# Kernel tuning notes

Hardware: AMD Instinct MI355X
Metric: run time of the kernel (lower is better)

## Reference

```python
import jax, jax.numpy as jnp
import numpy as np

B, T, C = 1, 4096, 1024
N_HEAD = 16
HEAD_DIM = C // N_HEAD
SCALE = 1.0 / np.sqrt(HEAD_DIM).astype(np.float32)


def setup_inputs() -> dict:
    key = jax.random.key(0)
    k1, k2, k3 = jax.random.split(key, 3)
    x = jax.random.normal(k1, (B, T, C), dtype=jnp.float32)
    W_attn = jax.random.normal(k2, (C, 3 * C), dtype=jnp.float32) * 0.02
    b_attn = jnp.zeros((3 * C,), dtype=jnp.float32)
    W_proj = jax.random.normal(k3, (C, C), dtype=jnp.float32) * 0.02
    b_proj = jnp.zeros((C,), dtype=jnp.float32)
    return {"x": x, "W_attn": W_attn, "b_attn": b_attn, "W_proj": W_proj, "b_proj": b_proj}


def reference(x, W_attn, b_attn, W_proj, b_proj):
    Bq, Tq, Cq = x.shape
    qkv = x @ W_attn + b_attn                      # [B, T, 3C]
    q, k, v = jnp.split(qkv, 3, axis=-1)
    # split heads -> [B, H, T, D]
    def split_heads(t):
        return t.reshape(Bq, Tq, N_HEAD, HEAD_DIM).transpose(0, 2, 1, 3)
    q, k, v = split_heads(q), split_heads(k), split_heads(v)
    scores = jnp.einsum('bhqd,bhkd->bhqk', q, k) * SCALE  # [B, H, T, T]
    causal = jnp.tril(jnp.ones((Tq, Tq), dtype=bool))
    scores = jnp.where(causal[None, None], scores, jnp.float32(-jnp.inf))
    probs = jax.nn.softmax(scores, axis=-1)
    out = jnp.einsum('bhqk,bhkd->bhqd', probs, v)          # [B, H, T, D]
    out = out.transpose(0, 2, 1, 3).reshape(Bq, Tq, Cq)    # merge heads
    out = out @ W_proj + b_proj
    return out
```

## Files before the change

### kernel.cpp

```cpp
#include <hip/hip_runtime.h>
#include <hip/hip_bf16.h>


typedef unsigned short u16;
typedef u16 u16x4 __attribute__((ext_vector_type(4)));
typedef u16 u16x8 __attribute__((ext_vector_type(8)));
typedef __bf16 bf16x8 __attribute__((ext_vector_type(8)));
typedef float f32x4 __attribute__((ext_vector_type(4)));

#define T_SEQ 4096
#define C_DIM 1024
#define NH 16
#define HD 64
#define QSC 0.18033688f

static __device__ __forceinline__ u16 f2bf(float f) {
    __hip_bfloat16 h = __float2bfloat16(f);
    return __builtin_bit_cast(u16, h);
}

static __device__ __forceinline__ bf16x8 ldfr(const u16* base, int byteoff) {
    return __builtin_bit_cast(bf16x8, *(const u16x8*)(base + (byteoff >> 1)));
}

static __device__ __forceinline__ void gld_lds16(const void* g, void* l) {
    __builtin_amdgcn_global_load_lds((const __attribute__((address_space(1))) void*)g,
                                     (__attribute__((address_space(3))) void*)l, 16, 0, 0);
}

#define MFMA16(a, b, c) __builtin_amdgcn_mfma_f32_16x16x32_bf16((a), (b), (c), 0, 0, 0)


__global__ __launch_bounds__(256) void k_cvt_x(const float* __restrict__ x, u16* __restrict__ xb) {
    int i = (blockIdx.x * 256 + threadIdx.x) * 8;
    float4 a = *(const float4*)(x + i);
    float4 b = *(const float4*)(x + i + 4);
    u16x8 o;
    o[0] = f2bf(a.x); o[1] = f2bf(a.y); o[2] = f2bf(a.z); o[3] = f2bf(a.w);
    o[4] = f2bf(b.x); o[5] = f2bf(b.y); o[6] = f2bf(b.z); o[7] = f2bf(b.w);
    *(u16x8*)(xb + i) = o;
}

__global__ __launch_bounds__(256) void k_transpose_w(const float* __restrict__ src,
                                                     u16* __restrict__ dst, int R, int Cc) {
    __shared__ float tile[32][33];
    int bx = blockIdx.x * 32;
    int by = blockIdx.y * 32;
    int x = threadIdx.x, y = threadIdx.y;
#pragma unroll
    for (int i = 0; i < 32; i += 8)
        tile[y + i][x] = src[(by + y + i) * Cc + bx + x];
    __syncthreads();
#pragma unroll
    for (int i = 0; i < 32; i += 8)
        dst[(bx + y + i) * R + by + x] = f2bf(tile[x][y + i]);
}


template <int EPI>
__global__ __launch_bounds__(256) void k_gemm(const u16* __restrict__ A, const u16* __restrict__ Bt,
                                              const float* __restrict__ bias,
                                              u16* __restrict__ outQ, u16* __restrict__ outK,
                                              u16* __restrict__ outVt, float* __restrict__ outF,
                                              int kd, int nbx) {
    __shared__ u16 Al[128 * 64];
    __shared__ u16 Bl[128 * 64];
    const int tid = threadIdx.x;
    const int lane = tid & 63;
    const int wid = tid >> 6;
    const int wm = wid >> 1, wn = wid & 1;
    const int c = lane & 15, g = lane >> 4;
    const int nwg = gridDim.x;
    const int swzb = ((int)blockIdx.x & 7) * (nwg >> 3) + ((int)blockIdx.x >> 3);
    const int m0 = (swzb % nbx) * 128;
    const int n0 = (swzb / nbx) * 128;
    const int srow = lane >> 3;
    const int sxu = (((lane & 7) * 16) ^ (srow << 4)) >> 1;
    const int swa = (c & 7) << 4;

    f32x4 acc[4][4] = {};

    for (int k0 = 0; k0 < kd; k0 += 64) {
#pragma unroll
        for (int i = 0; i < 4; ++i) {
            const int ch = wid * 4 + i;
            const int row = ch * 8 + srow;
            gld_lds16(A + (m0 + row) * kd + k0 + sxu, &Al[ch * 512]);
            gld_lds16(Bt + (n0 + row) * kd + k0 + sxu, &Bl[ch * 512]);
        }
        __syncthreads();
        bf16x8 af[4][2], bfm[4][2];
#pragma unroll
        for (int mi = 0; mi < 4; ++mi) {
            const u16* p = Al + (wm * 64 + mi * 16 + c) * 64;
            af[mi][0] = ldfr(p, (16 * g) ^ swa);
            af[mi][1] = ldfr(p, (64 + 16 * g) ^ swa);
        }
#pragma unroll
        for (int ni = 0; ni < 4; ++ni) {
            const u16* p = Bl + (wn * 64 + ni * 16 + c) * 64;
            bfm[ni][0] = ldfr(p, (16 * g) ^ swa);
            bfm[ni][1] = ldfr(p, (64 + 16 * g) ^ swa);
        }
#pragma unroll
        for (int mi = 0; mi < 4; ++mi)
#pragma unroll
            for (int ni = 0; ni < 4; ++ni) {
                acc[mi][ni] = MFMA16(af[mi][0], bfm[ni][0], acc[mi][ni]);
                acc[mi][ni] = MFMA16(af[mi][1], bfm[ni][1], acc[mi][ni]);
            }
        __syncthreads();
    }

    const int mbase = m0 + wm * 64;
    const int nbase = n0 + wn * 64;
    if (EPI == 0) {
#pragma unroll
        for (int ni = 0; ni < 4; ++ni) {
            const int n = nbase + ni * 16 + c;
            const float bv = bias[n];
            const int part = n >> 10;
            const int nr = n & 1023;
            const int h = nr >> 6, d = nr & 63;
#pragma unroll
            for (int mi = 0; mi < 4; ++mi) {
                const int mrow = mbase + mi * 16 + g * 4;
                if (part == 2) {
                    u16x4 pk;
#pragma unroll
                    for (int r = 0; r < 4; ++r) pk[r] = f2bf(acc[mi][ni][r] + bv);
                    *(u16x4*)(outVt + (h * HD + d) * T_SEQ + mrow) = pk;
                } else if (part == 1) {
                    u16* dst = outK + h * T_SEQ * HD + d;
#pragma unroll
                    for (int r = 0; r < 4; ++r) dst[(mrow + r) * HD] = f2bf(acc[mi][ni][r] + bv);
                } else {
                    u16* dst = outQ + h * T_SEQ * HD + d;
#pragma unroll
                    for (int r = 0; r < 4; ++r) dst[(mrow + r) * HD] = f2bf((acc[mi][ni][r] + bv) * QSC);
                }
            }
        }
    } else {
#pragma unroll
        for (int ni = 0; ni < 4; ++ni) {
            const int n = nbase + ni * 16 + c;
            const float bv = bias[n];
#pragma unroll
            for (int mi = 0; mi < 4; ++mi) {
                const int mrow = mbase + mi * 16 + g * 4;
#pragma unroll
                for (int r = 0; r < 4; ++r)
                    outF[(mrow + r) * C_DIM + n] = acc[mi][ni][r] + bv;
            }
        }
    }
}


static __device__ __forceinline__ void p_gen(f32x4 s[4], int qabs, int kv0, int g,
                                             bool domask, bf16x8 pa[2]) {
    if (domask) {
#pragma unroll
        for (int tau = 0; tau < 4; ++tau) {
            const int kb = kv0 + 32 * (tau >> 1) + 4 * (tau & 1) + 8 * g;
#pragma unroll
            for (int r = 0; r < 4; ++r)
                if (kb + r > qabs) s[tau][r] = -3e38f;
        }
    }
    u16 pb[4][4];
#pragma unroll
    for (int tau = 0; tau < 4; ++tau)
#pragma unroll
        for (int r = 0; r < 4; ++r)
            pb[tau][r] = f2bf(__builtin_amdgcn_exp2f(s[tau][r]));
    const u16x8 p0 = {pb[0][0], pb[0][1], pb[0][2], pb[0][3], pb[1][0], pb[1][1], pb[1][2], pb[1][3]};
    const u16x8 p1 = {pb[2][0], pb[2][1], pb[2][2], pb[2][3], pb[3][0], pb[3][1], pb[3][2], pb[3][3]};
    pa[0] = __builtin_bit_cast(bf16x8, p0);
    pa[1] = __builtin_bit_cast(bf16x8, p1);
}

__global__ __launch_bounds__(128) void k_flash(const u16* __restrict__ Qg, const u16* __restrict__ Kg,
                                               const u16* __restrict__ Vtg, u16* __restrict__ Oa,
                                               unsigned* __restrict__ cnt) {
    __shared__ u16 sm[2][2][4096];
    volatile unsigned* jw = (volatile unsigned*)&sm[0][0][0];

    const int tid = threadIdx.x;
    const int lane = tid & 63;
    const int wid = tid >> 6;
    const int c = lane & 15, g = lane >> 4;
    const int srow = lane >> 3;
    const int sxu = (((lane & 7) * 16) ^ (srow << 4)) >> 1;

    const u16x8 onespat = {0x3F80, 0x3F80, 0x3F80, 0x3F80, 0x3F80, 0x3F80, 0x3F80, 0x3F80};
    const bf16x8 onesf = __builtin_bit_cast(bf16x8, onespat);

    for (;;) {
        if (tid == 0) *jw = atomicAdd(cnt, 1u);
        __syncthreads();
        const unsigned j = *jw;
        __syncthreads();
        if (j >= 1024u) break;

        const int qb = 63 - (int)(j >> 4);
        const int head = (int)(j & 15u);
        const int q0w = qb * 64 + wid * 32;
        const int nt = qb + 1;

        const u16* Qh = Qg + head * (T_SEQ * HD);
        const u16* Kh = Kg + head * (T_SEQ * HD);
        const u16* Vh = Vtg + head * (HD * T_SEQ);

        bf16x8 qf[2][2];
#pragma unroll
        for (int h = 0; h < 2; ++h)
#pragma unroll
            for (int dc = 0; dc < 2; ++dc)
                qf[h][dc] = __builtin_bit_cast(
                    bf16x8, *(const u16x8*)(Qh + (q0w + 16 * h + c) * HD + dc * 32 + 8 * g));

        f32x4 o0[4] = {}, o1[4] = {}, ol0 = {}, ol1 = {};

#pragma unroll
        for (int i = 0; i < 4; ++i) {
            const int ch = wid * 4 + i;
            gld_lds16(Kh + (ch * 8 + srow) * HD + sxu, &sm[0][0][ch * 512]);
            gld_lds16(Vh + (ch * 8 + srow) * T_SEQ + sxu, &sm[0][1][ch * 512]);
        }
        __syncthreads();

        for (int t = 0; t < nt; ++t) {
            const int cur = t & 1;
            const int kv0 = t * 64;
            if (t + 1 < nt) {
                const int kvn = kv0 + 64;
#pragma unroll
                for (int i = 0; i < 4; ++i) {
                    const int ch = wid * 4 + i;
                    gld_lds16(Kh + (kvn + ch * 8 + srow) * HD + sxu, &sm[cur ^ 1][0][ch * 512]);
                    gld_lds16(Vh + (ch * 8 + srow) * T_SEQ + kvn + sxu, &sm[cur ^ 1][1][ch * 512]);
                }
            }
            const u16* Kl = &sm[cur][0][0];
            const u16* Vl = &sm[cur][1][0];
            f32x4 s0[4], s1[4];
            __builtin_amdgcn_s_setprio(1);
#pragma unroll
            for (int tau = 0; tau < 4; ++tau) {
                const int prow = 32 * (tau >> 1) + 4 * (tau & 1) + 8 * (c >> 2) + (c & 3);
                const int sw = (prow & 7) << 4;
                const u16* kb = Kl + prow * 64;
                const bf16x8 k0 = ldfr(kb, (16 * g) ^ sw);
                const bf16x8 k1 = ldfr(kb, (64 + 16 * g) ^ sw);
                f32x4 z0 = {}, z1 = {};
                z0 = MFMA16(k0, qf[0][0], z0);
                s0[tau] = MFMA16(k1, qf[0][1], z0);
                z1 = MFMA16(k0, qf[1][0], z1);
                s1[tau] = MFMA16(k1, qf[1][1], z1);
            }
            __builtin_amdgcn_s_setprio(0);
            const bool dm0 = (kv0 + 63) > (q0w);
            const bool dm1 = (kv0 + 63) > (q0w + 16);
            bf16x8 pa0[2], pa1[2];
            p_gen(s0, q0w + c, kv0, g, dm0, pa0);
            p_gen(s1, q0w + 16 + c, kv0, g, dm1, pa1);
            const int swv = (c & 7) << 4;
            __builtin_amdgcn_s_setprio(1);
#pragma unroll
            for (int n = 0; n < 4; ++n) {
                const u16* vb = Vl + (n * 16 + c) * 64;
                const bf16x8 v0 = ldfr(vb, (16 * g) ^ swv);
                const bf16x8 v1 = ldfr(vb, (64 + 16 * g) ^ swv);
                o0[n] = MFMA16(v0, pa0[0], o0[n]);
                o0[n] = MFMA16(v1, pa0[1], o0[n]);
                o1[n] = MFMA16(v0, pa1[0], o1[n]);
                o1[n] = MFMA16(v1, pa1[1], o1[n]);
            }
            ol0 = MFMA16(onesf, pa0[0], ol0);
            ol0 = MFMA16(onesf, pa0[1], ol0);
            ol1 = MFMA16(onesf, pa1[0], ol1);
            ol1 = MFMA16(onesf, pa1[1], ol1);
            __builtin_amdgcn_s_setprio(0);
            __syncthreads();
        }

        const float li0 = 1.0f / ol0[0], li1 = 1.0f / ol1[0];
#pragma unroll
        for (int n = 0; n < 4; ++n) {
            u16x4 w0, w1;
#pragma unroll
            for (int r = 0; r < 4; ++r) {
                w0[r] = f2bf(o0[n][r] * li0);
                w1[r] = f2bf(o1[n][r] * li1);
            }
            *(u16x4*)(Oa + (q0w + c) * C_DIM + head * HD + n * 16 + 4 * g) = w0;
            *(u16x4*)(Oa + (q0w + 16 + c) * C_DIM + head * HD + n * 16 + 4 * g) = w1;
        }
        __syncthreads();
    }
}


extern "C" void kernel_launch(void* const* d_in, const int* in_sizes, int n_in,
                              void* d_out, int out_size, void* d_ws, size_t ws_size,
                              hipStream_t stream) {
    const float* x      = (const float*)d_in[0];
    const float* W_attn = (const float*)d_in[1];
    const float* b_attn = (const float*)d_in[2];
    const float* W_proj = (const float*)d_in[3];
    const float* b_proj = (const float*)d_in[4];
    float* out = (float*)d_out;

    char* ws = (char*)d_ws;
    u16* xb  = (u16*)(ws);
    u16* Wat = (u16*)(ws + (8u << 20));
    u16* Wpt = (u16*)(ws + (14u << 20));
    u16* Qb  = (u16*)(ws + (16u << 20));
    u16* Kb  = (u16*)(ws + (24u << 20));
    u16* Vtb = (u16*)(ws + (32u << 20));
    u16* Ab  = (u16*)(ws + (40u << 20));

    unsigned* cnt = (unsigned*)d_out;
    hipMemsetAsync(cnt, 0, 4, stream);

    k_cvt_x<<<2048, 256, 0, stream>>>(x, xb);
    k_transpose_w<<<dim3(96, 32), dim3(32, 8), 0, stream>>>(W_attn, Wat, 1024, 3072);
    k_transpose_w<<<dim3(32, 32), dim3(32, 8), 0, stream>>>(W_proj, Wpt, 1024, 1024);
    k_gemm<0><<<768, 256, 0, stream>>>(xb, Wat, b_attn, Qb, Kb, Vtb, nullptr, 1024, 32);
    k_flash<<<1280, 128, 0, stream>>>(Qb, Kb, Vtb, Ab, cnt);
    k_gemm<1><<<256, 256, 0, stream>>>(Ab, Wpt, b_proj, nullptr, nullptr, nullptr, out, 1024, 32);
}
```

Measured before the change: 173.1 us.

## Split long causal attention rows across KV chunks and add combine kernel

Causal query blocks are split into up to four KV-range chunks depending on their length, giving 2560 work items instead of 1024 for the persistent flash kernel. Each chunk writes unnormalized fp32 partial outputs and row sums to a workspace. A new combine kernel sums the partials, normalizes them and writes the bf16 attention output. The aim is to shorten the critical path set by the longest query blocks, at the cost of extra fp32 partial traffic and one more kernel launch.

```diff
diff --git a/kernel.cpp b/kernel.cpp
--- a/kernel.cpp
+++ b/kernel.cpp
@@ -13,6 +13,7 @@
 #define NH 16
 #define HD 64
 #define QSC 0.18033688f
+#define NJOBS 2560
 
 static __device__ __forceinline__ u16 f2bf(float f) {
     __hip_bfloat16 h = __float2bfloat16(f);
@@ -182,7 +183,8 @@
 }
 
 __global__ __launch_bounds__(128) void k_flash(const u16* __restrict__ Qg, const u16* __restrict__ Kg,
-                                               const u16* __restrict__ Vtg, u16* __restrict__ Oa,
+                                               const u16* __restrict__ Vtg,
+                                               float* __restrict__ part, float* __restrict__ lpart,
                                                unsigned* __restrict__ cnt) {
     __shared__ u16 sm[2][2][4096];
     volatile unsigned* jw = (volatile unsigned*)&sm[0][0][0];
@@ -202,12 +204,21 @@
         __syncthreads();
         const unsigned j = *jw;
         __syncthreads();
-        if (j >= 1024u) break;
-
-        const int qb = 63 - (int)(j >> 4);
+        if (j >= (unsigned)NJOBS) break;
+
         const int head = (int)(j & 15u);
+        const int idx = (int)(j >> 4);
+        int qb, ch, nc;
+        if (idx < 64)       { qb = 63 - (idx >> 2); ch = idx & 3; nc = 4; }
+        else if (idx < 112) { const int t = idx - 64;  qb = 47 - t / 3;    ch = t % 3; nc = 3; }
+        else if (idx < 144) { const int t = idx - 112; qb = 31 - (t >> 1); ch = t & 1; nc = 2; }
+        else                { qb = 15 - (idx - 144); ch = 0; nc = 1; }
+        const int ntile = qb + 1;
+        const int cbase = ntile / nc, crem = ntile % nc;
+        const int len = cbase + (ch < crem ? 1 : 0);
+        const int start = ch * cbase + (ch < crem ? ch : crem);
+
         const int q0w = qb * 64 + wid * 32;
-        const int nt = qb + 1;
 
         const u16* Qh = Qg + head * (T_SEQ * HD);
         const u16* Kh = Kg + head * (T_SEQ * HD);
@@ -223,24 +234,27 @@
 
         f32x4 o0[4] = {}, o1[4] = {}, ol0 = {}, ol1 = {};
 
-#pragma unroll
-        for (int i = 0; i < 4; ++i) {
-            const int ch = wid * 4 + i;
-            gld_lds16(Kh + (ch * 8 + srow) * HD + sxu, &sm[0][0][ch * 512]);
-            gld_lds16(Vh + (ch * 8 + srow) * T_SEQ + sxu, &sm[0][1][ch * 512]);
-        }
-        __syncthreads();
-
-        for (int t = 0; t < nt; ++t) {
+        {
+            const int kvs = start * 64;
+#pragma unroll
+            for (int i = 0; i < 4; ++i) {
+                const int chk = wid * 4 + i;
+                gld_lds16(Kh + (kvs + chk * 8 + srow) * HD + sxu, &sm[0][0][chk * 512]);
+                gld_lds16(Vh + (chk * 8 + srow) * T_SEQ + kvs + sxu, &sm[0][1][chk * 512]);
+            }
+        }
+        __syncthreads();
+
+        for (int t = 0; t < len; ++t) {
             const int cur = t & 1;
-            const int kv0 = t * 64;
-            if (t + 1 < nt) {
+            const int kv0 = (start + t) * 64;
+            if (t + 1 < len) {
                 const int kvn = kv0 + 64;
 #pragma unroll
                 for (int i = 0; i < 4; ++i) {
-                    const int ch = wid * 4 + i;
-                    gld_lds16(Kh + (kvn + ch * 8 + srow) * HD + sxu, &sm[cur ^ 1][0][ch * 512]);
-                    gld_lds16(Vh + (ch * 8 + srow) * T_SEQ + kvn + sxu, &sm[cur ^ 1][1][ch * 512]);
+                    const int chk = wid * 4 + i;
+                    gld_lds16(Kh + (kvn + chk * 8 + srow) * HD + sxu, &sm[cur ^ 1][0][chk * 512]);
+                    gld_lds16(Vh + (chk * 8 + srow) * T_SEQ + kvn + sxu, &sm[cur ^ 1][1][chk * 512]);
                 }
             }
             const u16* Kl = &sm[cur][0][0];
@@ -286,20 +300,56 @@
             __syncthreads();
         }
 
-        const float li0 = 1.0f / ol0[0], li1 = 1.0f / ol1[0];
+        float* slot = part + (size_t)((unsigned)(head * 160 + idx)) * 4096u;
+        float* lsl = lpart + (head * 160 + idx) * 64;
+        const int ql0 = wid * 32 + c;
 #pragma unroll
         for (int n = 0; n < 4; ++n) {
-            u16x4 w0, w1;
-#pragma unroll
-            for (int r = 0; r < 4; ++r) {
-                w0[r] = f2bf(o0[n][r] * li0);
-                w1[r] = f2bf(o1[n][r] * li1);
-            }
-            *(u16x4*)(Oa + (q0w + c) * C_DIM + head * HD + n * 16 + 4 * g) = w0;
-            *(u16x4*)(Oa + (q0w + 16 + c) * C_DIM + head * HD + n * 16 + 4 * g) = w1;
-        }
-        __syncthreads();
-    }
+            *(f32x4*)(slot + ql0 * 64 + n * 16 + 4 * g) = o0[n];
+            *(f32x4*)(slot + (ql0 + 16) * 64 + n * 16 + 4 * g) = o1[n];
+        }
+        if (g == 0) {
+            lsl[ql0] = ol0[0];
+            lsl[ql0 + 16] = ol1[0];
+        }
+        __syncthreads();
+    }
+}
+
+
+__global__ __launch_bounds__(256) void k_combine(const float* __restrict__ part,
+                                                 const float* __restrict__ lpart,
+                                                 u16* __restrict__ Ab) {
+    const int head = blockIdx.x >> 6, qb = blockIdx.x & 63;
+    int nc, idx0;
+    if (qb >= 48)      { nc = 4; idx0 = (63 - qb) * 4; }
+    else if (qb >= 32) { nc = 3; idx0 = 64 + (47 - qb) * 3; }
+    else if (qb >= 16) { nc = 2; idx0 = 112 + (31 - qb) * 2; }
+    else               { nc = 1; idx0 = 144 + (15 - qb); }
+    const int base = head * 160 + idx0;
+
+    const int q = threadIdx.x >> 2;
+    const int s = threadIdx.x & 3;
+    f32x4 a[4] = {};
+    float l = 0.f;
+    for (int i = 0; i < nc; ++i) {
+        const float* sp = part + (size_t)(base + i) * 4096u + q * 64 + s * 16;
+#pragma unroll
+        for (int r = 0; r < 4; ++r) a[r] += *(const f32x4*)(sp + 4 * r);
+        l += lpart[(base + i) * 64 + q];
+    }
+    const float li = 1.0f / l;
+    u16x8 w0, w1;
+#pragma unroll
+    for (int r = 0; r < 4; ++r) {
+        w0[r] = f2bf(a[0][r] * li);
+        w0[r + 4] = f2bf(a[1][r] * li);
+        w1[r] = f2bf(a[2][r] * li);
+        w1[r + 4] = f2bf(a[3][r] * li);
+    }
+    u16* dst = Ab + (qb * 64 + q) * C_DIM + head * HD + s * 16;
+    *(u16x8*)dst = w0;
+    *(u16x8*)(dst + 8) = w1;
 }
 
 
@@ -314,13 +364,15 @@
     float* out = (float*)d_out;
 
     char* ws = (char*)d_ws;
-    u16* xb  = (u16*)(ws);
-    u16* Wat = (u16*)(ws + (8u << 20));
-    u16* Wpt = (u16*)(ws + (14u << 20));
-    u16* Qb  = (u16*)(ws + (16u << 20));
-    u16* Kb  = (u16*)(ws + (24u << 20));
-    u16* Vtb = (u16*)(ws + (32u << 20));
-    u16* Ab  = (u16*)(ws + (40u << 20));
+    u16* xb    = (u16*)(ws);
+    u16* Wat   = (u16*)(ws + (8u << 20));
+    u16* Wpt   = (u16*)(ws + (14u << 20));
+    u16* Qb    = (u16*)(ws + (16u << 20));
+    u16* Kb    = (u16*)(ws + (24u << 20));
+    u16* Vtb   = (u16*)(ws + (32u << 20));
+    float* prt = (float*)(ws + (40u << 20));
+    float* lpt = (float*)(ws + (80u << 20));
+    u16* Ab    = xb;
 
     unsigned* cnt = (unsigned*)d_out;
     hipMemsetAsync(cnt, 0, 4, stream);
@@ -329,6 +381,7 @@
     k_transpose_w<<<dim3(96, 32), dim3(32, 8), 0, stream>>>(W_attn, Wat, 1024, 3072);
     k_transpose_w<<<dim3(32, 32), dim3(32, 8), 0, stream>>>(W_proj, Wpt, 1024, 1024);
     k_gemm<0><<<768, 256, 0, stream>>>(xb, Wat, b_attn, Qb, Kb, Vtb, nullptr, 1024, 32);
-    k_flash<<<1280, 128, 0, stream>>>(Qb, Kb, Vtb, Ab, cnt);
+    k_flash<<<1280, 128, 0, stream>>>(Qb, Kb, Vtb, prt, lpt, cnt);
+    k_combine<<<1024, 256, 0, stream>>>(prt, lpt, Ab);
     k_gemm<1><<<256, 256, 0, stream>>>(Ab, Wpt, b_proj, nullptr, nullptr, nullptr, out, 1024, 32);
 }
```

Measured after the change: 180.3 us. +4.1%, slower.
